# Performance work log

Measured on AMD Instinct MI355X. Metric: run time of the kernel, lower is better.

## Reference

```python
import jax, jax.numpy as jnp
import numpy as np

B, S, D = 4, 2048, 1024
P = 2
N_FEAT = 16          # n_feature_know
N_REST = 16          # n_restore_know
R = 128              # knowledge_rank
D_SPACE = 64


def setup_inputs() -> dict:
    key = jax.random.key(0)
    ks = jax.random.split(key, 6)
    x = jax.random.normal(ks[0], (B, S, D), dtype=jnp.float32)
    # per-token routing weights for each of P feature paths, in [0,1)
    feature_paths = jax.random.uniform(ks[1], (P, B, S, N_FEAT), dtype=jnp.float32)
    f_know = jax.random.normal(ks[2], (N_FEAT, D, R), dtype=jnp.float32) * 0.02
    r_know = jax.random.normal(ks[3], (N_REST, R, D), dtype=jnp.float32) * 0.02
    feature_emb = jax.random.normal(ks[4], (N_FEAT, D_SPACE), dtype=jnp.float32)
    W_router = jax.random.normal(ks[5], (D_SPACE + R, N_REST), dtype=jnp.float32) * 0.05
    return {"x": x, "feature_paths": feature_paths, "f_know": f_know,
            "r_know": r_know, "feature_emb": feature_emb, "W_router": W_router}


def reference(x, feature_paths, f_know, r_know, feature_emb, W_router):
    # Feature projection into all N low-rank banks: [B,S,N,R]
    all_h = jnp.einsum('bsd,ndr->bsnr', x, f_know)
    # Weighted sum over banks per path: [P,B,S,R]
    h_all = jnp.einsum('bsnr,pbsn->pbsr', all_h, feature_paths)
    # Context for restore routing: [P,B,S,D_SPACE]
    neuron_ctx = jnp.einsum('pbsn,nd->pbsd', feature_paths, feature_emb)
    # restore_input = cat([neuron_ctx, h]) -> router -> softmax restore weights
    restore_input = jnp.concatenate([neuron_ctx, h_all], axis=-1)  # [P,B,S,D_SPACE+R]
    logits = jnp.einsum('pbsc,cn->pbsn', restore_input, W_router)
    w = jax.nn.softmax(logits, axis=-1)                            # [P,B,S,N_REST]
    # Restore + per-token weighted combine, summed over P paths: [B,S,D]
    output = jnp.einsum('pbsr,nrd,pbsn->bsd', h_all, r_know, w)
    restore_aux_loss = jnp.float32(0.0)
    return output, restore_aux_loss
```

## Files before the change

kernel.cpp:

```cpp
#include <hip/hip_runtime.h>

typedef __attribute__((ext_vector_type(4))) float f32x4;
typedef __bf16 bf16x8 __attribute__((ext_vector_type(8)));
typedef unsigned short ushort_t;

#define T_TOK 8192
#define DIM   1024
#define NRCOL 2048

#define LGKM0() asm volatile("s_waitcnt lgkmcnt(0)" ::: "memory")
#define VMW(n)  asm volatile("s_waitcnt vmcnt(" #n ")" ::: "memory")
#define SB0()   __builtin_amdgcn_sched_barrier(0)
#define BAR()   __builtin_amdgcn_s_barrier()

static __device__ __forceinline__ unsigned short f2bf(float f) {
  unsigned int u = __builtin_bit_cast(unsigned int, f);
  u += 0x7fffu + ((u >> 16) & 1u);
  return (unsigned short)(u >> 16);
}
static __device__ __forceinline__ float bfbits2f(unsigned int lo16) {
  return __builtin_bit_cast(float, lo16 << 16);
}
static __device__ __forceinline__ void gload16(const void* g, void* l) {
  __builtin_amdgcn_global_load_lds((const __attribute__((address_space(1))) void*)g,
                                   (__attribute__((address_space(3))) void*)l, 16, 0, 0);
}

__global__ __launch_bounds__(256) void cvt_f32_bf16(const float* __restrict__ in,
                                                    unsigned short* __restrict__ out,
                                                    int n4) {
  int i = blockIdx.x * 256 + threadIdx.x;
  const int stride = gridDim.x * 256;
  const float4* in4 = (const float4*)in;
  uint2* o4 = (uint2*)out;
  for (; i < n4; i += stride) {
    float4 v = in4[i];
    uint2 o;
    o.x = (unsigned)f2bf(v.x) | ((unsigned)f2bf(v.y) << 16);
    o.y = (unsigned)f2bf(v.z) | ((unsigned)f2bf(v.w) << 16);
    o4[i] = o;
  }
}

__global__ __launch_bounds__(256) void tcvt(const float* __restrict__ src,
                                            unsigned short* __restrict__ dst,
                                            int rows, int cols,
                                            long sstride, long dstride) {
  src += (size_t)blockIdx.z * sstride;
  dst += (size_t)blockIdx.z * dstride;
  __shared__ float tile[32][33];
  const int tx = threadIdx.x & 31, ty = threadIdx.x >> 5;
  const int r0 = blockIdx.y * 32, c0 = blockIdx.x * 32;
  #pragma unroll
  for (int i = 0; i < 32; i += 8)
    tile[ty + i][tx] = src[(size_t)(r0 + ty + i) * cols + c0 + tx];
  __syncthreads();
  #pragma unroll
  for (int i = 0; i < 32; i += 8)
    dst[(size_t)(c0 + ty + i) * rows + r0 + tx] = f2bf(tile[tx][ty + i]);
}

template<int BN, bool OUT_BF16>
__global__ __launch_bounds__(512) void gemm8(const ushort_t* __restrict__ A,
                                             const ushort_t* __restrict__ Bt,
                                             void* __restrict__ Cp,
                                             int N, int K) {
  constexpr int NF = BN / 64;
  constexpr int BR = BN / 64;
  constexpr int LPT = 4 + BR;
  __shared__ ushort_t As[2][256 * 64];
  __shared__ ushort_t Bs[2][BN * 64];

  const int tid = threadIdx.x;
  const int nx = gridDim.x;
  const int orig = blockIdx.y * nx + blockIdx.x;
  const int q = (nx * gridDim.y) >> 3;
  const int swz = (orig & 7) * q + (orig >> 3);
  const int bx = swz % nx, by = swz / nx;

  const int lane = tid & 63, wv = tid >> 6;
  const int wm = wv >> 2, wn = wv & 3;
  const int lrow = lane & 15, lk = lane >> 4;

  const ushort_t* Ab = A + (size_t)by * 256 * K;
  const ushort_t* Bb = Bt + (size_t)bx * BN * K;

  auto stage = [&](int c, int kt) {
    #pragma unroll
    for (int r = 0; r < 4; ++r) {
      const int off = r * 8192 + tid * 16;
      const int row = off >> 7;
      const int ch = ((off >> 4) & 7) ^ (row & 7);
      gload16(Ab + (size_t)row * K + kt * 64 + ch * 8, (void*)&As[c][off >> 1]);
    }
    #pragma unroll
    for (int r = 0; r < BR; ++r) {
      const int off = r * 8192 + tid * 16;
      const int row = off >> 7;
      const int ch = ((off >> 4) & 7) ^ (row & 7);
      gload16(Bb + (size_t)row * K + kt * 64 + ch * 8, (void*)&Bs[c][off >> 1]);
    }
  };

  f32x4 acc[8][NF];
  #pragma unroll
  for (int m = 0; m < 8; ++m)
    #pragma unroll
    for (int n = 0; n < NF; ++n)
      acc[m][n] = (f32x4){0.f, 0.f, 0.f, 0.f};

  const int nt = K >> 6;
  stage(0, 0);
  stage(1, 1);
  if constexpr (LPT == 8) VMW(8); else VMW(6);
  SB0(); BAR(); SB0();

  for (int t = 0; t < nt; ++t) {
    const int c = t & 1;
    bf16x8 av[8][2], bv[NF][2];
    #pragma unroll
    for (int m = 0; m < 8; ++m)
      #pragma unroll
      for (int ks = 0; ks < 2; ++ks) {
        const int row = wm * 128 + m * 16 + lrow;
        const int ch = (ks * 4 + lk) ^ (row & 7);
        av[m][ks] = *(const bf16x8*)&As[c][row * 64 + ch * 8];
      }
    #pragma unroll
    for (int n = 0; n < NF; ++n)
      #pragma unroll
      for (int ks = 0; ks < 2; ++ks) {
        const int row = wn * (BN / 4) + n * 16 + lrow;
        const int ch = (ks * 4 + lk) ^ (row & 7);
        bv[n][ks] = *(const bf16x8*)&Bs[c][row * 64 + ch * 8];
      }
    LGKM0();
    SB0();
    BAR();
    SB0();
    if (t + 2 < nt) stage(c, t + 2);
    __builtin_amdgcn_s_setprio(1);
    #pragma unroll
    for (int ks = 0; ks < 2; ++ks)
      #pragma unroll
      for (int m = 0; m < 8; ++m)
        #pragma unroll
        for (int n = 0; n < NF; ++n)
          acc[m][n] = __builtin_amdgcn_mfma_f32_16x16x32_bf16(av[m][ks], bv[n][ks], acc[m][n], 0, 0, 0);
    __builtin_amdgcn_s_setprio(0);
    SB0();
    if (t + 2 < nt) { if constexpr (LPT == 8) VMW(8); else VMW(6); }
    else if (t + 1 < nt) VMW(0);
    SB0();
    BAR();
    SB0();
  }

  #pragma unroll
  for (int m = 0; m < 8; ++m) {
    const int row0 = by * 256 + wm * 128 + m * 16 + lk * 4;
    #pragma unroll
    for (int n = 0; n < NF; ++n) {
      const int col = bx * BN + wn * (BN / 4) + n * 16 + lrow;
      #pragma unroll
      for (int j = 0; j < 4; ++j) {
        const size_t idx = (size_t)(row0 + j) * N + col;
        if constexpr (OUT_BF16) ((ushort_t*)Cp)[idx] = f2bf(acc[m][n][j]);
        else                    ((float*)Cp)[idx] = acc[m][n][j];
      }
    }
  }
}

__global__ __launch_bounds__(256) void middle_kernel(const unsigned short* __restrict__ AH,
                                                     const float* __restrict__ fp,
                                                     const float* __restrict__ femb,
                                                     const float* __restrict__ Wr,
                                                     unsigned short* __restrict__ Mout,
                                                     float* __restrict__ auxout) {
  __shared__ float G[16][16];
  __shared__ float hs[4][2][128];
  __shared__ float wsm[4][2][16];
  const int tid = threadIdx.x;
  {
    const int n = tid >> 4, j = tid & 15;
    float s = 0.f;
    #pragma unroll
    for (int ds = 0; ds < 64; ++ds) s += femb[n * 64 + ds] * Wr[ds * 16 + j];
    G[n][j] = s;
  }
  const int wv = tid >> 6, l = tid & 63;
  const int t = blockIdx.x * 4 + wv;

  float p0[16], p1[16];
  #pragma unroll
  for (int n = 0; n < 16; ++n) {
    p0[n] = fp[t * 16 + n];
    p1[n] = fp[T_TOK * 16 + t * 16 + n];
  }

  float h00 = 0.f, h01 = 0.f, h10 = 0.f, h11 = 0.f;
  const unsigned short* ahrow = AH + (size_t)t * NRCOL;
  #pragma unroll
  for (int n = 0; n < 16; ++n) {
    const unsigned int v = *(const unsigned int*)(ahrow + n * 128 + 2 * l);
    const float a0 = bfbits2f(v & 0xffffu);
    const float a1 = bfbits2f(v >> 16);
    h00 += a0 * p0[n]; h01 += a1 * p0[n];
    h10 += a0 * p1[n]; h11 += a1 * p1[n];
  }
  hs[wv][0][2 * l] = h00; hs[wv][0][2 * l + 1] = h01;
  hs[wv][1][2 * l] = h10; hs[wv][1][2 * l + 1] = h11;
  __syncthreads();

  if (l < 32) {
    const int p = l >> 4, j = l & 15;
    float s = 0.f;
    #pragma unroll
    for (int n = 0; n < 16; ++n) s += (p ? p1[n] : p0[n]) * G[n][j];
    for (int r = 0; r < 128; ++r) s += hs[wv][p][r] * Wr[(64 + r) * 16 + j];
    float mx = s;
    #pragma unroll
    for (int d = 1; d < 16; d <<= 1) mx = fmaxf(mx, __shfl_xor(mx, d, 64));
    const float e = __expf(s - mx);
    float sum = e;
    #pragma unroll
    for (int d = 1; d < 16; d <<= 1) sum += __shfl_xor(sum, d, 64);
    wsm[wv][p][j] = e / sum;
  }
  __syncthreads();

  unsigned short* mrow = Mout + (size_t)t * NRCOL;
  #pragma unroll
  for (int n = 0; n < 16; ++n) {
    const float w0 = wsm[wv][0][n], w1 = wsm[wv][1][n];
    const float m0 = w0 * h00 + w1 * h10;
    const float m1 = w0 * h01 + w1 * h11;
    const unsigned int pk = (unsigned)f2bf(m0) | ((unsigned)f2bf(m1) << 16);
    *(unsigned int*)(mrow + n * 128 + 2 * l) = pk;
  }
  if (blockIdx.x == 0 && tid == 0) auxout[0] = 0.f;
}

extern "C" void kernel_launch(void* const* d_in, const int* in_sizes, int n_in,
                              void* d_out, int out_size, void* d_ws, size_t ws_size,
                              hipStream_t stream) {
  const float* x    = (const float*)d_in[0];
  const float* fp   = (const float*)d_in[1];
  const float* fk   = (const float*)d_in[2];
  const float* rk   = (const float*)d_in[3];
  const float* femb = (const float*)d_in[4];
  const float* Wr   = (const float*)d_in[5];
  float* out = (float*)d_out;

  char* ws = (char*)d_ws;
  unsigned short* Xbf = (unsigned short*)ws;
  unsigned short* W1t = (unsigned short*)(ws + 16u * 1024 * 1024);
  unsigned short* Mb  = (unsigned short*)ws;
  unsigned short* W2t = (unsigned short*)(ws + 32u * 1024 * 1024);
  unsigned short* AH  = (unsigned short*)(ws + 36u * 1024 * 1024);

  cvt_f32_bf16<<<2048, 256, 0, stream>>>(x, Xbf, (T_TOK * DIM) / 4);
  tcvt<<<dim3(128 / 32, 1024 / 32, 16), 256, 0, stream>>>(fk, W1t, 1024, 128,
                                                          1024L * 128, 128L * 1024);
  tcvt<<<dim3(1024 / 32, 2048 / 32, 1), 256, 0, stream>>>(rk, W2t, 2048, 1024, 0, 0);
  gemm8<256, true><<<dim3(NRCOL / 256, T_TOK / 256), 512, 0, stream>>>(Xbf, W1t, AH,
                                                                       NRCOL, DIM);
  middle_kernel<<<T_TOK / 4, 256, 0, stream>>>(AH, fp, femb, Wr, Mb, out + 8388608);
  gemm8<128, false><<<dim3(DIM / 128, T_TOK / 256), 512, 0, stream>>>(Mb, W2t, out,
                                                                      DIM, NRCOL);
}
```

Baseline: 120.0 us.

## Replace GEMM with triple-buffered 256x128 tile, split-phase prefetch kernel

```diff
diff --git a/kernel.cpp b/kernel.cpp
--- a/kernel.cpp
+++ b/kernel.cpp
@@ -60,17 +60,13 @@
     dst[(size_t)(c0 + ty + i) * rows + r0 + tx] = f2bf(tile[tx][ty + i]);
 }
 
-template<int BN, bool OUT_BF16>
-__global__ __launch_bounds__(512) void gemm8(const ushort_t* __restrict__ A,
+template<bool OUT_BF16>
+__global__ __launch_bounds__(512) void gemm3(const ushort_t* __restrict__ A,
                                              const ushort_t* __restrict__ Bt,
                                              void* __restrict__ Cp,
                                              int N, int K) {
-  constexpr int NF = BN / 64;
-  constexpr int BR = BN / 64;
-  constexpr int LPT = 4 + BR;
-  __shared__ ushort_t As[2][256 * 64];
-  __shared__ ushort_t Bs[2][BN * 64];
-
+  __shared__ ushort_t As[3][256 * 64];
+  __shared__ ushort_t Bs[3][128 * 64];
   const int tid = threadIdx.x;
   const int nx = gridDim.x;
   const int orig = blockIdx.y * nx + blockIdx.x;
@@ -79,89 +75,107 @@
   const int bx = swz % nx, by = swz / nx;
 
   const int lane = tid & 63, wv = tid >> 6;
-  const int wm = wv >> 2, wn = wv & 3;
+  const int wm = wv >> 1, wn = wv & 1;
   const int lrow = lane & 15, lk = lane >> 4;
 
   const ushort_t* Ab = A + (size_t)by * 256 * K;
-  const ushort_t* Bb = Bt + (size_t)bx * BN * K;
-
-  auto stage = [&](int c, int kt) {
-    #pragma unroll
-    for (int r = 0; r < 4; ++r) {
-      const int off = r * 8192 + tid * 16;
-      const int row = off >> 7;
-      const int ch = ((off >> 4) & 7) ^ (row & 7);
-      gload16(Ab + (size_t)row * K + kt * 64 + ch * 8, (void*)&As[c][off >> 1]);
-    }
-    #pragma unroll
-    for (int r = 0; r < BR; ++r) {
-      const int off = r * 8192 + tid * 16;
-      const int row = off >> 7;
-      const int ch = ((off >> 4) & 7) ^ (row & 7);
-      gload16(Bb + (size_t)row * K + kt * 64 + ch * 8, (void*)&Bs[c][off >> 1]);
-    }
+  const ushort_t* Bb = Bt + (size_t)bx * 128 * K;
+
+  auto stageA = [&](int s, int kt, int r) {
+    const int off = r * 8192 + tid * 16;
+    const int row = off >> 7;
+    const int ch = ((off >> 4) & 7) ^ (row & 7);
+    gload16(Ab + (size_t)row * K + kt * 64 + ch * 8, (void*)&As[s][off >> 1]);
   };
-
-  f32x4 acc[8][NF];
-  #pragma unroll
-  for (int m = 0; m < 8; ++m)
-    #pragma unroll
-    for (int n = 0; n < NF; ++n)
+  auto stageB = [&](int s, int kt, int r) {
+    const int off = r * 8192 + tid * 16;
+    const int row = off >> 7;
+    const int ch = ((off >> 4) & 7) ^ (row & 7);
+    gload16(Bb + (size_t)row * K + kt * 64 + ch * 8, (void*)&Bs[s][off >> 1]);
+  };
+
+  f32x4 acc[4][4];
+  #pragma unroll
+  for (int m = 0; m < 4; ++m)
+    #pragma unroll
+    for (int n = 0; n < 4; ++n)
       acc[m][n] = (f32x4){0.f, 0.f, 0.f, 0.f};
 
   const int nt = K >> 6;
-  stage(0, 0);
-  stage(1, 1);
-  if constexpr (LPT == 8) VMW(8); else VMW(6);
-  SB0(); BAR(); SB0();
+  #pragma unroll
+  for (int r = 0; r < 4; ++r) stageA(0, 0, r);
+  #pragma unroll
+  for (int r = 0; r < 2; ++r) stageB(0, 0, r);
+  #pragma unroll
+  for (int r = 0; r < 4; ++r) stageA(1, 1, r);
+  #pragma unroll
+  for (int r = 0; r < 2; ++r) stageB(1, 1, r);
+  VMW(6); SB0(); BAR(); SB0();
 
   for (int t = 0; t < nt; ++t) {
-    const int c = t & 1;
-    bf16x8 av[8][2], bv[NF][2];
-    #pragma unroll
-    for (int m = 0; m < 8; ++m)
+    const int s = t % 3;
+    const int s2 = (t + 2) % 3;
+    const bool pf = (t + 2) < nt;
+    bf16x8 av[4][2], bv[4][2];
+    #pragma unroll
+    for (int m = 0; m < 2; ++m)
       #pragma unroll
       for (int ks = 0; ks < 2; ++ks) {
-        const int row = wm * 128 + m * 16 + lrow;
-        const int ch = (ks * 4 + lk) ^ (row & 7);
-        av[m][ks] = *(const bf16x8*)&As[c][row * 64 + ch * 8];
-      }
-    #pragma unroll
-    for (int n = 0; n < NF; ++n)
+        const int r = wm * 64 + m * 16 + lrow;
+        const int ch = (ks * 4 + lk) ^ (r & 7);
+        av[m][ks] = *(const bf16x8*)&As[s][r * 64 + ch * 8];
+      }
+    #pragma unroll
+    for (int n = 0; n < 4; ++n)
       #pragma unroll
       for (int ks = 0; ks < 2; ++ks) {
-        const int row = wn * (BN / 4) + n * 16 + lrow;
-        const int ch = (ks * 4 + lk) ^ (row & 7);
-        bv[n][ks] = *(const bf16x8*)&Bs[c][row * 64 + ch * 8];
-      }
-    LGKM0();
-    SB0();
-    BAR();
-    SB0();
-    if (t + 2 < nt) stage(c, t + 2);
+        const int r = wn * 64 + n * 16 + lrow;
+        const int ch = (ks * 4 + lk) ^ (r & 7);
+        bv[n][ks] = *(const bf16x8*)&Bs[s][r * 64 + ch * 8];
+      }
+    if (pf) { stageA(s2, t + 2, 0); stageA(s2, t + 2, 1); stageB(s2, t + 2, 0); }
+    SB0(); BAR(); LGKM0(); SB0();
     __builtin_amdgcn_s_setprio(1);
     #pragma unroll
     for (int ks = 0; ks < 2; ++ks)
       #pragma unroll
-      for (int m = 0; m < 8; ++m)
+      for (int m = 0; m < 2; ++m)
         #pragma unroll
-        for (int n = 0; n < NF; ++n)
+        for (int n = 0; n < 4; ++n)
+          acc[m][n] = __builtin_amdgcn_mfma_f32_16x16x32_bf16(av[m][ks], bv[n][ks], acc[m][n], 0, 0, 0);
+    __builtin_amdgcn_s_setprio(0);
+    SB0(); BAR(); SB0();
+    #pragma unroll
+    for (int m = 2; m < 4; ++m)
+      #pragma unroll
+      for (int ks = 0; ks < 2; ++ks) {
+        const int r = wm * 64 + m * 16 + lrow;
+        const int ch = (ks * 4 + lk) ^ (r & 7);
+        av[m][ks] = *(const bf16x8*)&As[s][r * 64 + ch * 8];
+      }
+    if (pf) { stageA(s2, t + 2, 2); stageA(s2, t + 2, 3); stageB(s2, t + 2, 1); }
+    SB0(); BAR(); LGKM0(); SB0();
+    __builtin_amdgcn_s_setprio(1);
+    #pragma unroll
+    for (int ks = 0; ks < 2; ++ks)
+      #pragma unroll
+      for (int m = 2; m < 4; ++m)
+        #pragma unroll
+        for (int n = 0; n < 4; ++n)
           acc[m][n] = __builtin_amdgcn_mfma_f32_16x16x32_bf16(av[m][ks], bv[n][ks], acc[m][n], 0, 0, 0);
     __builtin_amdgcn_s_setprio(0);
     SB0();
-    if (t + 2 < nt) { if constexpr (LPT == 8) VMW(8); else VMW(6); }
-    else if (t + 1 < nt) VMW(0);
-    SB0();
-    BAR();
-    SB0();
-  }
-
-  #pragma unroll
-  for (int m = 0; m < 8; ++m) {
-    const int row0 = by * 256 + wm * 128 + m * 16 + lk * 4;
-    #pragma unroll
-    for (int n = 0; n < NF; ++n) {
-      const int col = bx * BN + wn * (BN / 4) + n * 16 + lrow;
+    if (pf) { VMW(6); }
+    else if (t + 1 < nt) { VMW(0); }
+    SB0(); BAR(); SB0();
+  }
+
+  #pragma unroll
+  for (int m = 0; m < 4; ++m) {
+    const int row0 = by * 256 + wm * 64 + m * 16 + lk * 4;
+    #pragma unroll
+    for (int n = 0; n < 4; ++n) {
+      const int col = bx * 128 + wn * 64 + n * 16 + lrow;
       #pragma unroll
       for (int j = 0; j < 4; ++j) {
         const size_t idx = (size_t)(row0 + j) * N + col;
@@ -264,9 +278,9 @@
   tcvt<<<dim3(128 / 32, 1024 / 32, 16), 256, 0, stream>>>(fk, W1t, 1024, 128,
                                                           1024L * 128, 128L * 1024);
   tcvt<<<dim3(1024 / 32, 2048 / 32, 1), 256, 0, stream>>>(rk, W2t, 2048, 1024, 0, 0);
-  gemm8<256, true><<<dim3(NRCOL / 256, T_TOK / 256), 512, 0, stream>>>(Xbf, W1t, AH,
-                                                                       NRCOL, DIM);
+  gemm3<true><<<dim3(NRCOL / 128, T_TOK / 256), 512, 0, stream>>>(Xbf, W1t, AH,
+                                                                  NRCOL, DIM);
   middle_kernel<<<T_TOK / 4, 256, 0, stream>>>(AH, fp, femb, Wr, Mb, out + 8388608);
-  gemm8<128, false><<<dim3(DIM / 128, T_TOK / 256), 512, 0, stream>>>(Mb, W2t, out,
-                                                                      DIM, NRCOL);
-}
+  gemm3<false><<<dim3(DIM / 128, T_TOK / 256), 512, 0, stream>>>(Mb, W2t, out,
+                                                                 DIM, NRCOL);
+}
```

Measured after the change: 126.9 us. 1.06x slower.
